# Optimization experiments

Hardware: AMD Instinct MI355X
Metric: run time of the kernel (lower is better)

The kernel has to match this reference:

```python
import jax, jax.numpy as jnp
import numpy as np

NC = 80          # num classes
NBINS = 16       # DFL bins = reg_max_bbox_loss + 1
REG_MAX = 15     # BboxLoss reg_max (m.reg_max - 1)
GAMMA = 1.5      # focal gamma (h['fl_gamma'])
ALPHA = 0.25     # focal alpha
BOX_W, CLS_W, DFL_W = 7.5, 0.5, 1.5
LEVELS = [(80, 80), (40, 40), (20, 20)]  # 640x640 image, strides 8/16/32


def make_anchor_points():
    pts = []
    for h, w in LEVELS:
        ys, xs = np.meshgrid(np.arange(h) + 0.5, np.arange(w) + 0.5, indexing='ij')
        pts.append(np.stack([xs.ravel(), ys.ravel()], -1))
    return jnp.asarray(np.concatenate(pts, 0), jnp.float32)  # (8400, 2)


def setup_inputs() -> dict:
    B, A = 32, 8400
    key = jax.random.key(0)
    k = jax.random.split(key, 6)
    anchor_points = make_anchor_points()
    pred_dist = jax.random.normal(k[0], (B, A, 4 * NBINS), jnp.float32)
    pred_scores = jax.random.normal(k[1], (B, A, NC), jnp.float32)
    fg_mask = jax.random.uniform(k[2], (B, A)) < 0.05
    # valid xyxy targets around each anchor -> ltrb in (0.5, 6) < REG_MAX - 0.01
    off1 = jax.random.uniform(k[3], (B, A, 2), minval=0.5, maxval=6.0)
    off2 = jax.random.uniform(k[4], (B, A, 2), minval=0.5, maxval=6.0)
    target_bboxes = jnp.concatenate([anchor_points - off1, anchor_points + off2], -1)
    target_scores = jax.random.uniform(k[5], (B, A, NC)) * fg_mask[..., None].astype(jnp.float32)
    return dict(pred_dist=pred_dist, pred_scores=pred_scores,
                anchor_points=anchor_points, target_bboxes=target_bboxes,
                target_scores=target_scores, fg_mask=fg_mask)


def _ciou(b1, b2, eps=1e-7):
    # xyxy CIoU, matches ultralytics bbox_iou(xywh=False, CIoU=True)
    b1x1, b1y1, b1x2, b1y2 = b1[..., 0], b1[..., 1], b1[..., 2], b1[..., 3]
    b2x1, b2y1, b2x2, b2y2 = b2[..., 0], b2[..., 1], b2[..., 2], b2[..., 3]
    w1, h1 = b1x2 - b1x1, b1y2 - b1y1 + eps
    w2, h2 = b2x2 - b2x1, b2y2 - b2y1 + eps
    inter = (jnp.minimum(b1x2, b2x2) - jnp.maximum(b1x1, b2x1)).clip(0) * \
            (jnp.minimum(b1y2, b2y2) - jnp.maximum(b1y1, b2y1)).clip(0)
    union = w1 * h1 + w2 * h2 - inter + eps
    iou = inter / union
    cw = jnp.maximum(b1x2, b2x2) - jnp.minimum(b1x1, b2x1)
    ch = jnp.maximum(b1y2, b2y2) - jnp.minimum(b1y1, b2y1)
    c2 = cw * cw + ch * ch + eps
    rho2 = ((b2x1 + b2x2 - b1x1 - b1x2) ** 2 + (b2y1 + b2y2 - b1y1 - b1y2) ** 2) / 4.0
    v = (4.0 / (jnp.pi ** 2)) * (jnp.arctan(w2 / h2) - jnp.arctan(w1 / h1)) ** 2
    alpha = jax.lax.stop_gradient(v / (v - iou + (1.0 + eps)))  # torch.no_grad()
    return iou - (rho2 / c2 + v * alpha)


def _loss_core(pred_dist, pred_scores, anchor_points, target_bboxes, target_scores, fg_mask):
    B, A, _ = pred_scores.shape
    dt = pred_scores.dtype
    tss = jnp.maximum(target_scores.sum(), 1.0)  # target_scores_sum

    # ---- focal BCE (pos_weight=1) ----
    p = jax.nn.sigmoid(pred_scores)
    bce = target_scores * jax.nn.softplus(-pred_scores) + (1.0 - target_scores) * jax.nn.softplus(pred_scores)
    p_t = target_scores * p + (1.0 - target_scores) * (1.0 - p)
    alpha_f = target_scores * ALPHA + (1.0 - target_scores) * (1.0 - ALPHA)
    loss_cls = (bce * alpha_f * (1.0 - p_t) ** GAMMA).sum() / tss

    # ---- bbox decode (DFL expectation) ----
    proj = jnp.arange(NBINS, dtype=dt)
    logits = pred_dist.reshape(B, A, 4, NBINS)
    dist = jax.nn.softmax(logits, axis=-1) @ proj                     # (B,A,4) ltrb
    pred_bboxes = jnp.concatenate([anchor_points - dist[..., :2],
                                   anchor_points + dist[..., 2:]], -1)

    fg = fg_mask.astype(dt)
    bbox_weight = target_scores.sum(-1) * fg                          # masked weight (B,A)

    # ---- CIoU loss (mask replaces masked_select) ----
    iou = _ciou(pred_bboxes, target_bboxes)
    loss_iou = ((1.0 - iou) * bbox_weight).sum() / tss

    # ---- DFL loss: left/right weighted cross-entropy ----
    target_ltrb = jnp.clip(jnp.concatenate([anchor_points - target_bboxes[..., :2],
                                            target_bboxes[..., 2:] - anchor_points], -1),
                           0.0, REG_MAX - 0.01)                       # (B,A,4)
    tl = jnp.floor(target_ltrb).astype(jnp.int32)
    tr = tl + 1
    wl = tr.astype(dt) - target_ltrb
    wr = 1.0 - wl
    logp = jax.nn.log_softmax(logits, axis=-1)                        # (B,A,4,NBINS)
    ce_l = -jnp.take_along_axis(logp, tl[..., None], axis=-1)[..., 0]
    ce_r = -jnp.take_along_axis(logp, tr[..., None], axis=-1)[..., 0]
    loss_dfl = (((ce_l * wl + ce_r * wr).mean(-1)) * bbox_weight).sum() / tss

    return jnp.stack([BOX_W * loss_iou, CLS_W * loss_cls, DFL_W * loss_dfl])


def reference(pred_dist, pred_scores, anchor_points, target_bboxes, target_scores, fg_mask):
    loss = _loss_core(pred_dist, pred_scores, anchor_points, target_bboxes, target_scores, fg_mask)
    return loss  # weighted [box, cls, dfl]; total = loss.sum()
```

## Files before the change

### kernel.cpp

```cpp
#include <hip/hip_runtime.h>
#include <math.h>

#define NC      80
#define A_TOT   8400
#define B_TOT   32
#define BA      (B_TOT * A_TOT)
#define NFLAT4  (BA * 20)
#define TILE4   128
#define NTILES  (NFLAT4 / TILE4)
#define NCHUNK  (BA / 64)
#define BLOCK   256
#define NB_TARGET 2100

__device__ __forceinline__ float wave_sum(float v) {
    #pragma unroll
    for (int off = 32; off > 0; off >>= 1) v += __shfl_down(v, off, 64);
    return v;
}

__device__ __forceinline__ float cls_bg_term(float x) {
    float e   = __expf(-fabsf(x));
    float ope = 1.0f + e;
    float lp  = __logf(ope);
    float sp  = fmaxf(x, 0.0f) + lp;
    float r   = __builtin_amdgcn_rcpf(ope);
    float p   = (x >= 0.0f) ? r : (1.0f - r);
    return 0.75f * sp * (p * __builtin_amdgcn_sqrtf(p));
}

__device__ __forceinline__ void gl_lds_1k(const float4* g, float4* l) {
    __builtin_amdgcn_global_load_lds(
        (const __attribute__((address_space(1))) void*)g,
        (__attribute__((address_space(3))) void*)l, 16, 0, 0);
}

__global__ __launch_bounds__(BLOCK) void loss_main(
    const float* __restrict__ pred_dist,
    const float* __restrict__ pred_scores,
    const float* __restrict__ anchor_points,
    const float* __restrict__ target_bboxes,
    const float* __restrict__ target_scores,
    const int* __restrict__ fgmask,
    float* __restrict__ partials,
    int nb, int fgb)
{
    __shared__ float4 stage[4][2][TILE4];
    __shared__ float red[4][4];

    const int tid  = threadIdx.x;
    const int lane = tid & 63;
    const int wid  = tid >> 6;

    const float4* ps4 = (const float4*)pred_scores;
    const float4* ts4 = (const float4*)target_scores;
    const float4* tb4 = (const float4*)target_bboxes;

    float cls_acc = 0.0f, iou_acc = 0.0f, dfl_acc = 0.0f, ts_acc = 0.0f;

    if ((int)blockIdx.x < fgb) {
        const int fstride = fgb * 4;
        for (int c = blockIdx.x * 4 + wid; c < NCHUNK; c += fstride) {
            const int abase = c * 64;
            const int myfg = fgmask[abase + lane];
            unsigned long long m = __ballot(myfg != 0);

            int gc = -1; float xc = 0.0f;
            float4 tbc = make_float4(0,0,0,0), tsc = make_float4(0,0,0,0);
            float4 psc = make_float4(0,0,0,0);
            if (m) {
                int b = __ffsll((long long)m) - 1; m &= m - 1;
                gc = abase + b;
                xc  = pred_dist[gc * 64 + lane];
                tbc = tb4[gc];
                tsc = (lane < 20) ? ts4[gc * 20 + lane] : make_float4(0,0,0,0);
                psc = (lane >= 32 && lane < 52) ? ps4[gc * 20 + (lane - 32)]
                                                : make_float4(0,0,0,0);
            }
            while (gc >= 0) {
                int gn = -1; float xn = 0.0f;
                float4 tbn = make_float4(0,0,0,0), tsn = make_float4(0,0,0,0);
                float4 psn = make_float4(0,0,0,0);
                if (m) {
                    int b = __ffsll((long long)m) - 1; m &= m - 1;
                    gn = abase + b;
                    xn  = pred_dist[gn * 64 + lane];
                    tbn = tb4[gn];
                    tsn = (lane < 20) ? ts4[gn * 20 + lane] : make_float4(0,0,0,0);
                    psn = (lane >= 32 && lane < 52) ? ps4[gn * 20 + (lane - 32)]
                                                    : make_float4(0,0,0,0);
                }

                float w = tsc.x + tsc.y + tsc.z + tsc.w;
                #pragma unroll
                for (int off = 1; off < 64; off <<= 1) w += __shfl_xor(w, off, 64);

                float qx = __shfl(psc.x, lane + 32);
                float qy = __shfl(psc.y, lane + 32);
                float qz = __shfl(psc.z, lane + 32);
                float qw = __shfl(psc.w, lane + 32);
                if (lane < 20) {
                    float pxs[4] = {qx, qy, qz, qw};
                    float tvs[4] = {tsc.x, tsc.y, tsc.z, tsc.w};
                    #pragma unroll
                    for (int j = 0; j < 4; ++j) {
                        float x  = pxs[j];
                        float tv = tvs[j];
                        float e   = __expf(-fabsf(x));
                        float ope = 1.0f + e;
                        float lp  = __logf(ope);
                        float sp  = fmaxf(x, 0.0f) + lp;
                        float r   = __builtin_amdgcn_rcpf(ope);
                        float p   = (x >= 0.0f) ? r : (1.0f - r);
                        float bce = sp - tv * x;
                        float u   = fmaxf(fmaf(p, 1.0f - 2.0f * tv, tv), 0.0f);
                        float af  = 0.75f - 0.5f * tv;
                        float t1  = af * bce * (u * __builtin_amdgcn_sqrtf(u));
                        float t0  = 0.75f * sp * (p * __builtin_amdgcn_sqrtf(p));
                        cls_acc += t1 - t0;
                    }
                }

                const int a = gc % A_TOT;
                const float ax = anchor_points[2 * a];
                const float ay = anchor_points[2 * a + 1];
                const int side = lane >> 4;
                const int k    = lane & 15;
                const float x  = xc;

                float tval = (side == 0) ? ax - tbc.x :
                             (side == 1) ? ay - tbc.y :
                             (side == 2) ? tbc.z - ax : tbc.w - ay;
                float tcl = fminf(fmaxf(tval, 0.0f), 14.99f);
                int   tl  = (int)tcl;
                float wl  = (float)(tl + 1) - tcl;
                float wr  = 1.0f - wl;

                float mx = x;
                mx = fmaxf(mx, __shfl_xor(mx, 1));
                mx = fmaxf(mx, __shfl_xor(mx, 2));
                mx = fmaxf(mx, __shfl_xor(mx, 4));
                mx = fmaxf(mx, __shfl_xor(mx, 8));

                float ex = __expf(x - mx);
                float se = ex;
                float nu = (float)k * ex;
                float ls = ((k == tl) ? wl : (k == tl + 1) ? wr : 0.0f) * x;
                #pragma unroll
                for (int off = 1; off < 16; off <<= 1) {
                    se += __shfl_xor(se, off);
                    nu += __shfl_xor(nu, off);
                    ls += __shfl_xor(ls, off);
                }
                float dist = nu * __builtin_amdgcn_rcpf(se);
                float ce   = mx + __logf(se) - ls;

                float d0 = __shfl(dist, 0),  d1 = __shfl(dist, 16);
                float d2 = __shfl(dist, 32), d3 = __shfl(dist, 48);
                float c0 = __shfl(ce, 0),    c1 = __shfl(ce, 16);
                float c2 = __shfl(ce, 32),   c3 = __shfl(ce, 48);

                if (lane == 0) {
                    ts_acc  += w;
                    dfl_acc += 0.25f * (c0 + c1 + c2 + c3) * w;

                    const float eps = 1e-7f;
                    float px1 = ax - d0, py1 = ay - d1;
                    float px2 = ax + d2, py2 = ay + d3;
                    float w1 = px2 - px1, h1 = py2 - py1 + eps;
                    float w2 = tbc.z - tbc.x, h2 = tbc.w - tbc.y + eps;
                    float iw = fmaxf(fminf(px2, tbc.z) - fmaxf(px1, tbc.x), 0.0f);
                    float ih = fmaxf(fminf(py2, tbc.w) - fmaxf(py1, tbc.y), 0.0f);
                    float inter = iw * ih;
                    float uni = w1 * h1 + w2 * h2 - inter + eps;
                    float iou = inter / uni;
                    float cw = fmaxf(px2, tbc.z) - fminf(px1, tbc.x);
                    float ch = fmaxf(py2, tbc.w) - fminf(py1, tbc.y);
                    float c2d = cw * cw + ch * ch + eps;
                    float dx = tbc.x + tbc.z - px1 - px2;
                    float dy = tbc.y + tbc.w - py1 - py2;
                    float rho2 = (dx * dx + dy * dy) * 0.25f;
                    const float c4pi2 = 0.40528473456935109f;
                    float dat = atanf(w2 / h2) - atanf(w1 / h1);
                    float v = c4pi2 * dat * dat;
                    float alpha = v / (v - iou + (1.0f + eps));
                    float ciou = iou - (rho2 / c2d + v * alpha);
                    iou_acc += (1.0f - ciou) * w;
                }

                gc = gn; xc = xn; tbc = tbn; tsc = tsn; psc = psn;
            }
        }
    } else {
        const int dwid = (blockIdx.x - fgb) * 4 + wid;
        const int ndw  = (nb - fgb) * 4;
        if (dwid < NTILES) {
            float4* buf0 = stage[wid][0];
            float4* buf1 = stage[wid][1];
            const int nt = (NTILES - 1 - dwid) / ndw + 1;

            const float4* s0 = ps4 + (size_t)dwid * TILE4;
            gl_lds_1k(s0 + lane, buf0);
            gl_lds_1k(s0 + 64 + lane, buf0 + 64);
            const float4* s1 = (nt > 1) ? ps4 + (size_t)(dwid + ndw) * TILE4 : s0;
            gl_lds_1k(s1 + lane, buf1);
            gl_lds_1k(s1 + 64 + lane, buf1 + 64);

            for (int t = 0; t < nt; ++t) {
                asm volatile("s_waitcnt vmcnt(2)" ::: "memory");
                __builtin_amdgcn_sched_barrier(0);
                float4* cur = (t & 1) ? buf1 : buf0;
                float4 v0 = cur[lane];
                float4 v1 = cur[lane + 64];
                asm volatile("s_waitcnt lgkmcnt(0)" ::: "memory");
                __builtin_amdgcn_sched_barrier(0);
                int nx = (t + 2 < nt) ? (t + 2) : (nt - 1);
                const float4* sn = ps4 + (size_t)(dwid + (size_t)nx * ndw) * TILE4;
                gl_lds_1k(sn + lane, cur);
                gl_lds_1k(sn + 64 + lane, cur + 64);
                cls_acc += cls_bg_term(v0.x); cls_acc += cls_bg_term(v0.y);
                cls_acc += cls_bg_term(v0.z); cls_acc += cls_bg_term(v0.w);
                cls_acc += cls_bg_term(v1.x); cls_acc += cls_bg_term(v1.y);
                cls_acc += cls_bg_term(v1.z); cls_acc += cls_bg_term(v1.w);
            }
        }
    }

    float v0 = wave_sum(iou_acc);
    float v1 = wave_sum(cls_acc);
    float v2 = wave_sum(ts_acc);
    float v3 = wave_sum(dfl_acc);
    if (lane == 0) { red[0][wid] = v0; red[1][wid] = v1; red[2][wid] = v2; red[3][wid] = v3; }
    __syncthreads();
    if (tid == 0) {
        float r0 = 0, r1 = 0, r2 = 0, r3 = 0;
        #pragma unroll
        for (int i = 0; i < 4; ++i) { r0 += red[0][i]; r1 += red[1][i]; r2 += red[2][i]; r3 += red[3][i]; }
        partials[0 * nb + blockIdx.x] = r0;
        partials[1 * nb + blockIdx.x] = r1;
        partials[2 * nb + blockIdx.x] = r2;
        partials[3 * nb + blockIdx.x] = r3;
    }
}

__global__ __launch_bounds__(BLOCK) void loss_reduce(
    const float* __restrict__ partials, int nb, float* __restrict__ out)
{
    __shared__ float red[4][4];
    int tid = threadIdx.x;
    float s0 = 0, s1 = 0, s2 = 0, s3 = 0;
    for (int i = tid; i < nb; i += BLOCK) {
        s0 += partials[i];
        s1 += partials[nb + i];
        s2 += partials[2 * nb + i];
        s3 += partials[3 * nb + i];
    }
    s0 = wave_sum(s0); s1 = wave_sum(s1); s2 = wave_sum(s2); s3 = wave_sum(s3);
    int wid = tid >> 6;
    if ((tid & 63) == 0) { red[0][wid] = s0; red[1][wid] = s1; red[2][wid] = s2; red[3][wid] = s3; }
    __syncthreads();
    if (tid == 0) {
        float r0 = 0, r1 = 0, r2 = 0, r3 = 0;
        #pragma unroll
        for (int i = 0; i < 4; ++i) { r0 += red[0][i]; r1 += red[1][i]; r2 += red[2][i]; r3 += red[3][i]; }
        float tss = fmaxf(r2, 1.0f);
        out[0] = 7.5f * r0 / tss;
        out[1] = 0.5f * r1 / tss;
        out[2] = 1.5f * r3 / tss;
    }
}

extern "C" void kernel_launch(void* const* d_in, const int* in_sizes, int n_in,
                              void* d_out, int out_size, void* d_ws, size_t ws_size,
                              hipStream_t stream) {
    const float* pred_dist     = (const float*)d_in[0];
    const float* pred_scores   = (const float*)d_in[1];
    const float* anchor_points = (const float*)d_in[2];
    const float* target_bboxes = (const float*)d_in[3];
    const float* target_scores = (const float*)d_in[4];
    const int*   fgmask        = (const int*)d_in[5];

    int nb = (int)(ws_size / (4 * sizeof(float)));
    if (nb > NB_TARGET) nb = NB_TARGET;
    if (nb < 2) nb = 2;
    int fgb = nb / 2;
    if (fgb < 1) fgb = 1;

    float* partials = (float*)d_ws;
    loss_main<<<nb, BLOCK, 0, stream>>>(
        pred_dist, pred_scores, anchor_points, target_bboxes, target_scores,
        fgmask, partials, nb, fgb);
    loss_reduce<<<1, BLOCK, 0, stream>>>(partials, nb, (float*)d_out);
}
```

Baseline: 218.7 us.

## Split foreground and dense work across waves within each block

Instead of giving half the blocks to foreground anchors and half to dense background tiles, each block now uses wave 3 for foreground chunks and waves 0-2 for streaming pred_scores tiles. The grid is reduced, and the background focal term is rewritten to use one exp(-|x|/2) plus rsqrt, so sigmoid^1.5 comes from r^3 without a separate sqrt. This aims to balance the two kinds of work inside every CU and cut transcendental instructions per element. The cost is a different load balance: a single foreground wave per block may become the tail.

```diff
diff --git a/kernel.cpp b/kernel.cpp
--- a/kernel.cpp
+++ b/kernel.cpp
@@ -10,7 +10,7 @@
 #define NTILES  (NFLAT4 / TILE4)
 #define NCHUNK  (BA / 64)
 #define BLOCK   256
-#define NB_TARGET 2100
+#define NB_TARGET 1400
 
 __device__ __forceinline__ float wave_sum(float v) {
     #pragma unroll
@@ -19,13 +19,15 @@
 }
 
 __device__ __forceinline__ float cls_bg_term(float x) {
-    float e   = __expf(-fabsf(x));
-    float ope = 1.0f + e;
+    float t2  = __expf(-0.5f * fabsf(x));
+    float t   = t2 * t2;
+    float ope = 1.0f + t;
+    float r   = __builtin_amdgcn_rsqf(ope);
     float lp  = __logf(ope);
     float sp  = fmaxf(x, 0.0f) + lp;
-    float r   = __builtin_amdgcn_rcpf(ope);
-    float p   = (x >= 0.0f) ? r : (1.0f - r);
-    return 0.75f * sp * (p * __builtin_amdgcn_sqrtf(p));
+    float r3  = r * r * r;
+    float p15 = (x >= 0.0f) ? r3 : t * t2 * r3;
+    return 0.75f * sp * p15;
 }
 
 __device__ __forceinline__ void gl_lds_1k(const float4* g, float4* l) {
@@ -42,9 +44,9 @@
     const float* __restrict__ target_scores,
     const int* __restrict__ fgmask,
     float* __restrict__ partials,
-    int nb, int fgb)
+    int nb)
 {
-    __shared__ float4 stage[4][2][TILE4];
+    __shared__ float4 stage[3][2][TILE4];
     __shared__ float red[4][4];
 
     const int tid  = threadIdx.x;
@@ -57,9 +59,8 @@
 
     float cls_acc = 0.0f, iou_acc = 0.0f, dfl_acc = 0.0f, ts_acc = 0.0f;
 
-    if ((int)blockIdx.x < fgb) {
-        const int fstride = fgb * 4;
-        for (int c = blockIdx.x * 4 + wid; c < NCHUNK; c += fstride) {
+    if (wid == 3) {
+        for (int c = blockIdx.x; c < NCHUNK; c += nb) {
             const int abase = c * 64;
             const int myfg = fgmask[abase + lane];
             unsigned long long m = __ballot(myfg != 0);
@@ -105,17 +106,19 @@
                     for (int j = 0; j < 4; ++j) {
                         float x  = pxs[j];
                         float tv = tvs[j];
-                        float e   = __expf(-fabsf(x));
-                        float ope = 1.0f + e;
+                        float t2  = __expf(-0.5f * fabsf(x));
+                        float t   = t2 * t2;
+                        float ope = 1.0f + t;
+                        float r   = __builtin_amdgcn_rsqf(ope);
+                        float pp  = r * r;
+                        float p   = (x >= 0.0f) ? pp : (1.0f - pp);
                         float lp  = __logf(ope);
                         float sp  = fmaxf(x, 0.0f) + lp;
-                        float r   = __builtin_amdgcn_rcpf(ope);
-                        float p   = (x >= 0.0f) ? r : (1.0f - r);
                         float bce = sp - tv * x;
                         float u   = fmaxf(fmaf(p, 1.0f - 2.0f * tv, tv), 0.0f);
                         float af  = 0.75f - 0.5f * tv;
                         float t1  = af * bce * (u * __builtin_amdgcn_sqrtf(u));
-                        float t0  = 0.75f * sp * (p * __builtin_amdgcn_sqrtf(p));
+                        float t0  = cls_bg_term(x);
                         cls_acc += t1 - t0;
                     }
                 }
@@ -191,8 +194,8 @@
             }
         }
     } else {
-        const int dwid = (blockIdx.x - fgb) * 4 + wid;
-        const int ndw  = (nb - fgb) * 4;
+        const int dwid = (int)blockIdx.x * 3 + wid;
+        const int ndw  = nb * 3;
         if (dwid < NTILES) {
             float4* buf0 = stage[wid][0];
             float4* buf1 = stage[wid][1];
@@ -281,13 +284,11 @@
 
     int nb = (int)(ws_size / (4 * sizeof(float)));
     if (nb > NB_TARGET) nb = NB_TARGET;
-    if (nb < 2) nb = 2;
-    int fgb = nb / 2;
-    if (fgb < 1) fgb = 1;
+    if (nb < 1) nb = 1;
 
     float* partials = (float*)d_ws;
     loss_main<<<nb, BLOCK, 0, stream>>>(
         pred_dist, pred_scores, anchor_points, target_bboxes, target_scores,
-        fgmask, partials, nb, fgb);
+        fgmask, partials, nb);
     loss_reduce<<<1, BLOCK, 0, stream>>>(partials, nb, (float*)d_out);
 }
```

Result: slower. 232.4 us (+6.3%).
